# Kernel optimization log

Hardware: AMD Instinct MI355X
Metric: run time of the kernel (lower is better)

## Reference

```python
import jax, jax.numpy as jnp
import numpy as np

H = 128  # GRU hidden size

def gru_cell(x, h, Wih, Whh, bih, bhh):
    # torch GRU gate order: r, z, n
    gx = x @ Wih.T + bih          # (B, 3H)
    gh = h @ Whh.T + bhh          # (B, 3H)
    xr, xz, xn = jnp.split(gx, 3, axis=-1)
    hr, hz, hn = jnp.split(gh, 3, axis=-1)
    r = jax.nn.sigmoid(xr + hr)
    z = jax.nn.sigmoid(xz + hz)
    n = jnp.tanh(xn + r * hn)
    return (1.0 - z) * n + z * h

def conv2d(x, w, b, stride):
    y = jax.lax.conv_general_dilated(x, w, window_strides=(stride, stride), padding='VALID',
                                     dimension_numbers=('NCHW', 'OIHW', 'NCHW'))
    return y + b[None, :, None, None]

def setup_inputs() -> dict:
    key = jax.random.key(0)
    ks = jax.random.split(key, 20)
    B, T = 8192, 64
    s = lambda *sh: 0.1
    inp = {
        'cnn_states': jax.random.normal(ks[0], (B, 8, 8, 27), jnp.float32),
        'linears_states': jax.random.normal(ks[1], (B, T, 29), jnp.float32),
        'conv1_w': jax.random.normal(ks[2], (16, 27, 3, 3), jnp.float32) * 0.1,
        'conv1_b': jnp.zeros((16,), jnp.float32),
        'conv2_w': jax.random.normal(ks[3], (32, 16, 2, 2), jnp.float32) * 0.1,
        'conv2_b': jnp.zeros((32,), jnp.float32),
        'fc_w': jax.random.normal(ks[4], (128, 128), jnp.float32) * 0.1,
        'fc_b': jnp.zeros((128,), jnp.float32),
        'enc_Wih': jax.random.normal(ks[5], (3 * H, 29), jnp.float32) * 0.1,
        'enc_Whh': jax.random.normal(ks[6], (3 * H, H), jnp.float32) * 0.1,
        'enc_bih': jnp.zeros((3 * H,), jnp.float32),
        'enc_bhh': jnp.zeros((3 * H,), jnp.float32),
        'dec_Wih': jax.random.normal(ks[7], (3 * H, H), jnp.float32) * 0.1,
        'dec_Whh': jax.random.normal(ks[8], (3 * H, H), jnp.float32) * 0.1,
        'dec_bih': jnp.zeros((3 * H,), jnp.float32),
        'dec_bhh': jnp.zeros((3 * H,), jnp.float32),
        'dis_w': jax.random.normal(ks[9], (78, 256), jnp.float32) * 0.01,
        'dis_b': jnp.zeros((78,), jnp.float32),
        'value_w': jax.random.normal(ks[10], (1, 256), jnp.float32) * 0.1,
        'value_b': jnp.zeros((1,), jnp.float32),
    }
    return inp

def _forward(cnn_states, linears_states, conv1_w, conv1_b, conv2_w, conv2_b, fc_w, fc_b,
             enc_Wih, enc_Whh, enc_bih, enc_bhh, dec_Wih, dec_Whh, dec_bih, dec_bhh,
             dis_w, dis_b, value_w, value_b):
    B, T = linears_states.shape[0], linears_states.shape[1]
    # CNN encoder (NHWC -> NCHW)
    x = jnp.transpose(cnn_states, (0, 3, 1, 2))
    x = jax.nn.relu(conv2d(x, conv1_w, conv1_b, 2))   # (B,16,3,3)
    x = jax.nn.relu(conv2d(x, conv2_w, conv2_b, 1))   # (B,32,2,2)
    x = x.reshape(B, -1)                               # (B,128), CHW order matches torch Flatten
    z_cnn = jax.nn.relu(x @ fc_w.T + fc_b)             # (B,128)

    # encoder GRU over linears_states
    xs = jnp.transpose(linears_states, (1, 0, 2))      # (T,B,29)
    h0 = jnp.zeros((B, H), linears_states.dtype)
    def enc_step(h, xt):
        h2 = gru_cell(xt, h, enc_Wih, enc_Whh, enc_bih, enc_bhh)
        return h2, None
    h_enc, _ = jax.lax.scan(enc_step, h0, xs)

    x0 = jnp.zeros((B, H), linears_states.dtype)
    def dec_step(carry, _):
        xin, h = carry
        h2 = gru_cell(xin, h, dec_Wih, dec_Whh, dec_bih, dec_bhh)
        return (h2, h2), None
    (z_pn, _), _ = jax.lax.scan(dec_step, (x0, h_enc), None, length=T)

    pn = jnp.concatenate([z_cnn, z_pn], axis=1)        # (B,256)
    distris = pn @ dis_w.T + dis_b                     # (B,78)
    value = pn @ value_w.T + value_b                   # (B,1)
    return distris, value

def reference(cnn_states, linears_states, conv1_w, conv1_b, conv2_w, conv2_b, fc_w, fc_b,
              enc_Wih, enc_Whh, enc_bih, enc_bhh, dec_Wih, dec_Whh, dec_bih, dec_bhh,
              dis_w, dis_b, value_w, value_b):
    return _forward(cnn_states, linears_states, conv1_w, conv1_b, conv2_w, conv2_b, fc_w, fc_b,
                    enc_Wih, enc_Whh, enc_bih, enc_bhh, dec_Wih, dec_Whh, dec_bih, dec_bhh,
                    dis_w, dis_b, value_w, value_b)
```

## Files before the change

### kernel.cpp

```cpp
#include <hip/hip_runtime.h>

typedef _Float16 f16;
typedef _Float16 f16x8 __attribute__((ext_vector_type(8)));
typedef float f32x4 __attribute__((ext_vector_type(4)));

#define WS_EWIH 4194304
#define WS_EWHH 4218880
#define WS_DWC  4317184
#define WS_DWHH 4448256
#define WS_BIAS 4546560
#define WS_W1F  4550656
#define WS_W2F  4559872
#define WS_FCWF 4563968

static __device__ __forceinline__ f32x4 mfma16(f16x8 a, f16x8 b, f32x4 c) {
    return __builtin_amdgcn_mfma_f32_16x16x32_f16(a, b, c, 0, 0, 0);
}
static __device__ __forceinline__ float fexp2n(float x) {
    return __builtin_amdgcn_exp2f(x * -1.4426950408889634f);
}

__global__ void k_prep(const float* __restrict__ eWih, const float* __restrict__ eWhh,
                       const float* __restrict__ ebih, const float* __restrict__ ebhh,
                       const float* __restrict__ dWih, const float* __restrict__ dWhh,
                       const float* __restrict__ dbih, const float* __restrict__ dbhh,
                       const float* __restrict__ w1, const float* __restrict__ w2,
                       const float* __restrict__ fcw,
                       char* __restrict__ ws)
{
    f16* ewih = (f16*)(ws + WS_EWIH);
    f16* ewhh = (f16*)(ws + WS_EWHH);
    f16* dwc  = (f16*)(ws + WS_DWC);
    f16* dwhh = (f16*)(ws + WS_DWHH);
    float* bias = (float*)(ws + WS_BIAS);
    f16* w1f = (f16*)(ws + WS_W1F);
    f16* w2f = (f16*)(ws + WS_W2F);
    f16* fcwf = (f16*)(ws + WS_FCWF);
    const int total = 12288 + 49152 + 65536 + 49152 + 1024 + 4608 + 2048 + 16384;
    for (int i = blockIdx.x * 256 + threadIdx.x; i < total; i += gridDim.x * 256) {
        int j = i;
        if (j < 12288) { int g = j >> 5, k = j & 31;
            ewih[j] = (f16)((k < 29) ? eWih[g * 29 + k] : 0.0f); continue; }
        j -= 12288;
        if (j < 49152) { ewhh[j] = (f16)eWhh[j]; continue; }
        j -= 49152;
        if (j < 65536) { int row = j >> 7, k = j & 127; float v;
            if (row < 256)      v = dWih[row * 128 + k] + dWhh[row * 128 + k];
            else if (row < 384) v = dWih[row * 128 + k];
            else                v = dWhh[(row - 128) * 128 + k];
            dwc[j] = (f16)v; continue; }
        j -= 65536;
        if (j < 49152) { dwhh[j] = (f16)dWhh[j]; continue; }
        j -= 49152;
        if (j < 1024) {
            if (j < 256)        bias[j] = ebih[j] + ebhh[j];
            else if (j < 384)   bias[j] = ebih[j];
            else if (j < 512)   bias[j] = ebhh[j - 128];
            else if (j < 768)   bias[j] = dbih[j - 512] + dbhh[j - 512];
            else if (j < 896)   bias[j] = dbih[j - 512];
            else                bias[j] = dbhh[j - 640];
            continue; }
        j -= 1024;
        if (j < 4608) {
            int kk = j >> 9, rem = j & 511, co = rem >> 5, k = rem & 31;
            w1f[j] = (f16)((k < 27) ? w1[co * 243 + k * 9 + kk] : 0.0f); continue; }
        j -= 4608;
        if (j < 2048) {
            int s = j >> 10, rem = j & 1023, co = rem >> 5, k = rem & 31;
            int kk2 = 2 * s + (k >= 16), ci = k & 15;
            w2f[j] = (f16)w2[co * 64 + ci * 4 + kk2]; continue; }
        j -= 2048;
        fcwf[j] = (f16)fcw[j];
    }
}

__global__ __launch_bounds__(512, 2) void k_gru(
    const float* __restrict__ cin,
    const float* __restrict__ lin,
    const float* __restrict__ b1, const float* __restrict__ b2,
    const float* __restrict__ fcb,
    const char* __restrict__ ws,
    const float* __restrict__ dis_w, const float* __restrict__ dis_b,
    const float* __restrict__ value_w, const float* __restrict__ value_b,
    float* __restrict__ out)
{
    __shared__ __align__(16) char smem[55296];
    f16 (*h_s)[2][16][136]  = (f16(*)[2][16][136])(smem);
    f16 (*x_s)[2][16][32]   = (f16(*)[2][16][32])(smem + 17408);
    float (*pn_s)[264]      = (float(*)[264])(smem + 21504);
    f16 (*a1f)[9][24]       = (f16(*)[9][24])(smem);
    f16 (*vf)[136]          = (f16(*)[136])(smem + 8704);

    const int tid = threadIdx.x;
    const int wv = tid >> 6;
    const int lane = tid & 63;
    const int nl = lane & 15;
    const int quad = lane >> 4;
    const int j0 = wv * 16;
    const int row0 = blockIdx.x * 32;

    const f16* ewih = (const f16*)(ws + WS_EWIH);
    const f16* ewhh = (const f16*)(ws + WS_EWHH);
    const f16* dwc  = (const f16*)(ws + WS_DWC);
    const f16* dwhh = (const f16*)(ws + WS_DWHH);
    const float* bias = (const float*)(ws + WS_BIAS);
    const f16* w1f = (const f16*)(ws + WS_W1F);
    const f16* w2f = (const f16*)(ws + WS_W2F);
    const f16* fcwf = (const f16*)(ws + WS_FCWF);

    for (int g = 0; g < 2; g++) {
        const float* imgp = cin + (size_t)(row0 + g * 16 + nl) * 1728 + quad * 8;
        float b1v = b1[nl];
        for (int p = wv; p < 9; p += 8) {
            int oy = p / 3, ox = p % 3;
            f32x4 acc = {b1v, b1v, b1v, b1v};
            #pragma unroll
            for (int kk = 0; kk < 9; kk++) {
                f16x8 bw = *(const f16x8*)(w1f + (kk * 16 + nl) * 32 + quad * 8);
                int pix = (2 * oy + kk / 3) * 8 + (2 * ox + kk % 3);
                const float* s = imgp + pix * 27;
                f16x8 a;
                #pragma unroll
                for (int jj = 0; jj < 8; jj++) a[jj] = (f16)s[jj];
                acc = mfma16(a, bw, acc);
            }
            #pragma unroll
            for (int r = 0; r < 4; r++)
                a1f[quad * 4 + r][p][nl] = (f16)fmaxf(acc[r], 0.0f);
        }
        __syncthreads();
        {
            int pos = wv >> 1, nt = wv & 1;
            int y = pos >> 1, x = pos & 1;
            float bv = b2[nt * 16 + nl];
            f32x4 acc = {bv, bv, bv, bv};
            #pragma unroll
            for (int s = 0; s < 2; s++) {
                int kk2 = 2 * s + (quad >> 1);
                int pos1 = (y + (kk2 >> 1)) * 3 + (x + (kk2 & 1));
                f16x8 a = *(const f16x8*)(&a1f[nl][pos1][(quad & 1) * 8]);
                f16x8 b = *(const f16x8*)(w2f + ((size_t)s * 32 + nt * 16 + nl) * 32 + quad * 8);
                acc = mfma16(a, b, acc);
            }
            #pragma unroll
            for (int r = 0; r < 4; r++)
                vf[quad * 4 + r][(nt * 16 + nl) * 4 + (y * 2 + x)] = (f16)fmaxf(acc[r], 0.0f);
        }
        __syncthreads();
        {
            int o = wv * 16 + nl;
            float bv = fcb[o];
            f32x4 acc = {bv, bv, bv, bv};
            #pragma unroll
            for (int kt = 0; kt < 4; kt++) {
                f16x8 a = *(const f16x8*)(&vf[nl][kt * 32 + quad * 8]);
                f16x8 b = *(const f16x8*)(fcwf + o * 128 + kt * 32 + quad * 8);
                acc = mfma16(a, b, acc);
            }
            #pragma unroll
            for (int r = 0; r < 4; r++)
                pn_s[g * 16 + quad * 4 + r][o] = fmaxf(acc[r], 0.0f);
        }
        __syncthreads();
    }

    for (int i = tid; i < 2 * 2 * 16 * 136; i += 512) ((f16*)h_s)[i] = (f16)0.0f;

    const int rsw = (nl & 8) ? 16 : 0;
    const int wrow = quad * 4;
    const int wsw = (quad >= 2) ? 16 : 0;
    const int wcol = (j0 + nl + wsw) & 127;
    const int c0 = (quad * 8 + rsw) & 127;
    const int c1 = (32 + quad * 8 + rsw) & 127;
    const int c2 = (64 + quad * 8 + rsw) & 127;
    const int c3 = (96 + quad * 8 + rsw) & 127;

    float hoA[4], hoB[4];
    #pragma unroll
    for (int r = 0; r < 4; r++) { hoA[r] = 0.0f; hoB[r] = 0.0f; }

    const int xr = tid >> 5, xc = tid & 31;
    const bool xok = (xc < 29);
    const size_t lin_baseA = (size_t)(row0 + xr) * 1856 + xc;
    const size_t lin_baseB = (size_t)(row0 + 16 + xr) * 1856 + xc;

#define GATES(AR, AZ, AXN, AHN, HO, OB, TI, BR, BZ, BXN, BHN)                        \
        _Pragma("unroll")                                                            \
        for (int r = 0; r < 4; r++) {                                                \
            float ea = fexp2n((AR)[r]), eb = fexp2n((AZ)[r]);                        \
            float s1 = 1.0f + ea, s2 = 1.0f + eb;                                    \
            float R = __builtin_amdgcn_rcpf(s1 * s2);                                \
            float rg = s2 * R, zg = s1 * R;                                          \
            float ec = fexp2n(2.0f * ((AXN)[r] + rg * (AHN)[r]));                    \
            float ng = (1.0f - ec) * __builtin_amdgcn_rcpf(1.0f + ec);               \
            float h = ng + zg * ((HO)[r] - ng);                                      \
            (HO)[r] = h;                                                             \
            h_s[OB][TI][wrow + r][wcol] = (f16)h;                                    \
        }

    {
        float eb_r, eb_z, eb_xn, eb_hn;
        { int c = j0 + nl;
          eb_r = bias[c]; eb_z = bias[128 + c]; eb_xn = bias[256 + c]; eb_hn = bias[384 + c]; }
        f16x8 we_r[4], we_z[4], we_hn[4], we_xr, we_xz, we_xn;
        { int gr = j0 + nl;
          #pragma unroll
          for (int kt = 0; kt < 4; kt++) {
              we_r[kt]  = *(const f16x8*)(ewhh + gr * 128 + kt * 32 + quad * 8);
              we_z[kt]  = *(const f16x8*)(ewhh + (128 + gr) * 128 + kt * 32 + quad * 8);
              we_hn[kt] = *(const f16x8*)(ewhh + (256 + gr) * 128 + kt * 32 + quad * 8);
          }
          we_xr = *(const f16x8*)(ewih + gr * 32 + quad * 8);
          we_xz = *(const f16x8*)(ewih + (128 + gr) * 32 + quad * 8);
          we_xn = *(const f16x8*)(ewih + (256 + gr) * 32 + quad * 8);
        }

        float xvA = xok ? lin[lin_baseA] : 0.0f;
        float xvB = xok ? lin[lin_baseB] : 0.0f;

#define ENC_STEP(BUF, OBUF, TN)                                                      \
        do {                                                                         \
            x_s[BUF][0][xr][xc] = (f16)xvA;                                          \
            x_s[BUF][1][xr][xc] = (f16)xvB;                                          \
            __syncthreads();                                                         \
            f16x8 axA = *(const f16x8*)(&x_s[BUF][0][nl][quad * 8]);                 \
            f16x8 axB = *(const f16x8*)(&x_s[BUF][1][nl][quad * 8]);                 \
            f16x8 aA0 = *(const f16x8*)(&h_s[BUF][0][nl][c0]);                       \
            f16x8 aA1 = *(const f16x8*)(&h_s[BUF][0][nl][c1]);                       \
            f16x8 aA2 = *(const f16x8*)(&h_s[BUF][0][nl][c2]);                       \
            f16x8 aA3 = *(const f16x8*)(&h_s[BUF][0][nl][c3]);                       \
            f16x8 aB0 = *(const f16x8*)(&h_s[BUF][1][nl][c0]);                       \
            f16x8 aB1 = *(const f16x8*)(&h_s[BUF][1][nl][c1]);                       \
            f16x8 aB2 = *(const f16x8*)(&h_s[BUF][1][nl][c2]);                       \
            f16x8 aB3 = *(const f16x8*)(&h_s[BUF][1][nl][c3]);                       \
            if ((TN) < 64) {                                                         \
                xvA = xok ? lin[lin_baseA + (TN) * 29] : 0.0f;                       \
                xvB = xok ? lin[lin_baseB + (TN) * 29] : 0.0f;                       \
            }                                                                        \
            f32x4 aRA  = {eb_r, eb_r, eb_r, eb_r},   aRB  = aRA;                     \
            f32x4 aZA  = {eb_z, eb_z, eb_z, eb_z},   aZB  = aZA;                     \
            f32x4 aXNA = {eb_xn, eb_xn, eb_xn, eb_xn}, aXNB = aXNA;                  \
            f32x4 aHNA = {eb_hn, eb_hn, eb_hn, eb_hn}, aHNB = aHNA;                  \
            aRA  = mfma16(axA, we_xr, aRA);   aRB  = mfma16(axB, we_xr, aRB);        \
            aZA  = mfma16(axA, we_xz, aZA);   aZB  = mfma16(axB, we_xz, aZB);        \
            aXNA = mfma16(axA, we_xn, aXNA);  aXNB = mfma16(axB, we_xn, aXNB);       \
            aRA  = mfma16(aA0, we_r[0], aRA);  aRB  = mfma16(aB0, we_r[0], aRB);     \
            aRA  = mfma16(aA1, we_r[1], aRA);  aRB  = mfma16(aB1, we_r[1], aRB);     \
            aRA  = mfma16(aA2, we_r[2], aRA);  aRB  = mfma16(aB2, we_r[2], aRB);     \
            aRA  = mfma16(aA3, we_r[3], aRA);  aRB  = mfma16(aB3, we_r[3], aRB);     \
            aZA  = mfma16(aA0, we_z[0], aZA);  aZB  = mfma16(aB0, we_z[0], aZB);     \
            aZA  = mfma16(aA1, we_z[1], aZA);  aZB  = mfma16(aB1, we_z[1], aZB);     \
            aZA  = mfma16(aA2, we_z[2], aZA);  aZB  = mfma16(aB2, we_z[2], aZB);     \
            aZA  = mfma16(aA3, we_z[3], aZA);  aZB  = mfma16(aB3, we_z[3], aZB);     \
            aHNA = mfma16(aA0, we_hn[0], aHNA); aHNB = mfma16(aB0, we_hn[0], aHNB);  \
            aHNA = mfma16(aA1, we_hn[1], aHNA); aHNB = mfma16(aB1, we_hn[1], aHNB);  \
            aHNA = mfma16(aA2, we_hn[2], aHNA); aHNB = mfma16(aB2, we_hn[2], aHNB);  \
            aHNA = mfma16(aA3, we_hn[3], aHNA); aHNB = mfma16(aB3, we_hn[3], aHNB);  \
            GATES(aRA, aZA, aXNA, aHNA, hoA, OBUF, 0, , , , )                        \
            GATES(aRB, aZB, aXNB, aHNB, hoB, OBUF, 1, , , , )                        \
        } while (0)

        for (int t = 0; t < 64; t += 2) {
            ENC_STEP(0, 1, t + 1);
            ENC_STEP(1, 0, t + 2);
        }
#undef ENC_STEP
    }

    float db_r, db_z, db_xn, db_hn;
    { int c = j0 + nl;
      db_r = bias[512 + c]; db_z = bias[640 + c]; db_xn = bias[768 + c]; db_hn = bias[896 + c]; }

    {
        __syncthreads();
        f16x8 aA0 = *(const f16x8*)(&h_s[0][0][nl][c0]);
        f16x8 aA1 = *(const f16x8*)(&h_s[0][0][nl][c1]);
        f16x8 aA2 = *(const f16x8*)(&h_s[0][0][nl][c2]);
        f16x8 aA3 = *(const f16x8*)(&h_s[0][0][nl][c3]);
        f16x8 aB0 = *(const f16x8*)(&h_s[0][1][nl][c0]);
        f16x8 aB1 = *(const f16x8*)(&h_s[0][1][nl][c1]);
        f16x8 aB2 = *(const f16x8*)(&h_s[0][1][nl][c2]);
        f16x8 aB3 = *(const f16x8*)(&h_s[0][1][nl][c3]);
        int gr = j0 + nl;
        f32x4 aRA  = {db_r, db_r, db_r, db_r},   aRB  = aRA;
        f32x4 aZA  = {db_z, db_z, db_z, db_z},   aZB  = aZA;
        f32x4 aHNA = {db_hn, db_hn, db_hn, db_hn}, aHNB = aHNA;
        #pragma unroll
        for (int kt = 0; kt < 4; kt++) {
            f16x8 b0 = *(const f16x8*)(dwhh + gr * 128 + kt * 32 + quad * 8);
            f16x8 b1 = *(const f16x8*)(dwhh + (128 + gr) * 128 + kt * 32 + quad * 8);
            f16x8 b2 = *(const f16x8*)(dwhh + (256 + gr) * 128 + kt * 32 + quad * 8);
            f16x8 aA = (kt == 0) ? aA0 : (kt == 1) ? aA1 : (kt == 2) ? aA2 : aA3;
            f16x8 aB = (kt == 0) ? aB0 : (kt == 1) ? aB1 : (kt == 2) ? aB2 : aB3;
            aRA  = mfma16(aA, b0, aRA);   aRB  = mfma16(aB, b0, aRB);
            aZA  = mfma16(aA, b1, aZA);   aZB  = mfma16(aB, b1, aZB);
            aHNA = mfma16(aA, b2, aHNA);  aHNB = mfma16(aB, b2, aHNB);
        }
        #pragma unroll
        for (int r = 0; r < 4; r++) {
            float ea = fexp2n(aRA[r]), eb = fexp2n(aZA[r]);
            float s1 = 1.0f + ea, s2 = 1.0f + eb;
            float R = __builtin_amdgcn_rcpf(s1 * s2);
            float rg = s2 * R, zg = s1 * R;
            float ec = fexp2n(2.0f * (db_xn + rg * aHNA[r]));
            float ng = (1.0f - ec) * __builtin_amdgcn_rcpf(1.0f + ec);
            float h = ng + zg * (hoA[r] - ng);
            hoA[r] = h;
            h_s[1][0][wrow + r][wcol] = (f16)h;
        }
        #pragma unroll
        for (int r = 0; r < 4; r++) {
            float ea = fexp2n(aRB[r]), eb = fexp2n(aZB[r]);
            float s1 = 1.0f + ea, s2 = 1.0f + eb;
            float R = __builtin_amdgcn_rcpf(s1 * s2);
            float rg = s2 * R, zg = s1 * R;
            float ec = fexp2n(2.0f * (db_xn + rg * aHNB[r]));
            float ng = (1.0f - ec) * __builtin_amdgcn_rcpf(1.0f + ec);
            float h = ng + zg * (hoB[r] - ng);
            hoB[r] = h;
            h_s[1][1][wrow + r][wcol] = (f16)h;
        }
    }
    {
        f16x8 wd_r[4], wd_z[4], wd_xn[4], wd_hn[4];
        { int gr = j0 + nl;
          #pragma unroll
          for (int kt = 0; kt < 4; kt++) {
              wd_r[kt]  = *(const f16x8*)(dwc + gr * 128 + kt * 32 + quad * 8);
              wd_z[kt]  = *(const f16x8*)(dwc + (128 + gr) * 128 + kt * 32 + quad * 8);
              wd_xn[kt] = *(const f16x8*)(dwc + (256 + gr) * 128 + kt * 32 + quad * 8);
              wd_hn[kt] = *(const f16x8*)(dwc + (384 + gr) * 128 + kt * 32 + quad * 8);
          }
        }

#define DEC_STEP(BUF, OBUF)                                                          \
        do {                                                                         \
            __syncthreads();                                                         \
            f16x8 aA0 = *(const f16x8*)(&h_s[BUF][0][nl][c0]);                       \
            f16x8 aA1 = *(const f16x8*)(&h_s[BUF][0][nl][c1]);                       \
            f16x8 aA2 = *(const f16x8*)(&h_s[BUF][0][nl][c2]);                       \
            f16x8 aA3 = *(const f16x8*)(&h_s[BUF][0][nl][c3]);                       \
            f16x8 aB0 = *(const f16x8*)(&h_s[BUF][1][nl][c0]);                       \
            f16x8 aB1 = *(const f16x8*)(&h_s[BUF][1][nl][c1]);                       \
            f16x8 aB2 = *(const f16x8*)(&h_s[BUF][1][nl][c2]);                       \
            f16x8 aB3 = *(const f16x8*)(&h_s[BUF][1][nl][c3]);                       \
            f32x4 aRA  = {db_r, db_r, db_r, db_r},   aRB  = aRA;                     \
            f32x4 aZA  = {db_z, db_z, db_z, db_z},   aZB  = aZA;                     \
            f32x4 aXNA = {db_xn, db_xn, db_xn, db_xn}, aXNB = aXNA;                  \
            f32x4 aHNA = {db_hn, db_hn, db_hn, db_hn}, aHNB = aHNA;                  \
            aRA  = mfma16(aA0, wd_r[0], aRA);   aRB  = mfma16(aB0, wd_r[0], aRB);    \
            aRA  = mfma16(aA1, wd_r[1], aRA);   aRB  = mfma16(aB1, wd_r[1], aRB);    \
            aRA  = mfma16(aA2, wd_r[2], aRA);   aRB  = mfma16(aB2, wd_r[2], aRB);    \
            aRA  = mfma16(aA3, wd_r[3], aRA);   aRB  = mfma16(aB3, wd_r[3], aRB);    \
            aZA  = mfma16(aA0, wd_z[0], aZA);   aZB  = mfma16(aB0, wd_z[0], aZB);    \
            aZA  = mfma16(aA1, wd_z[1], aZA);   aZB  = mfma16(aB1, wd_z[1], aZB);    \
            aZA  = mfma16(aA2, wd_z[2], aZA);   aZB  = mfma16(aB2, wd_z[2], aZB);    \
            aZA  = mfma16(aA3, wd_z[3], aZA);   aZB  = mfma16(aB3, wd_z[3], aZB);    \
            aXNA = mfma16(aA0, wd_xn[0], aXNA); aXNB = mfma16(aB0, wd_xn[0], aXNB);  \
            aXNA = mfma16(aA1, wd_xn[1], aXNA); aXNB = mfma16(aB1, wd_xn[1], aXNB);  \
            aXNA = mfma16(aA2, wd_xn[2], aXNA); aXNB = mfma16(aB2, wd_xn[2], aXNB);  \
            aXNA = mfma16(aA3, wd_xn[3], aXNA); aXNB = mfma16(aB3, wd_xn[3], aXNB);  \
            aHNA = mfma16(aA0, wd_hn[0], aHNA); aHNB = mfma16(aB0, wd_hn[0], aHNB);  \
            aHNA = mfma16(aA1, wd_hn[1], aHNA); aHNB = mfma16(aB1, wd_hn[1], aHNB);  \
            aHNA = mfma16(aA2, wd_hn[2], aHNA); aHNB = mfma16(aB2, wd_hn[2], aHNB);  \
            aHNA = mfma16(aA3, wd_hn[3], aHNA); aHNB = mfma16(aB3, wd_hn[3], aHNB);  \
            GATES(aRA, aZA, aXNA, aHNA, hoA, OBUF, 0, , , , )                        \
            GATES(aRB, aZB, aXNB, aHNB, hoB, OBUF, 1, , , , )                        \
        } while (0)

        DEC_STEP(1, 0);
        for (int t = 2; t < 64; t += 2) {
            DEC_STEP(0, 1);
            DEC_STEP(1, 0);
        }
#undef DEC_STEP
#undef GATES
    }

    #pragma unroll
    for (int r = 0; r < 4; r++) {
        pn_s[wrow + r][128 + j0 + nl] = hoA[r];
        pn_s[16 + wrow + r][128 + j0 + nl] = hoB[r];
    }
    __syncthreads();

    const int rr = tid & 31, og = tid >> 5;
    const float4* pr4 = (const float4*)(&pn_s[rr][0]);
    for (int o = og; o < 79; o += 16) {
        const float* wrow_p = (o < 78) ? (dis_w + o * 256) : value_w;
        float acc = (o < 78) ? dis_b[o] : value_b[0];
        const float4* wr4 = (const float4*)wrow_p;
        #pragma unroll 8
        for (int k = 0; k < 64; k++) {
            float4 a = wr4[k], b = pr4[k];
            acc += a.x * b.x + a.y * b.y + a.z * b.z + a.w * b.w;
        }
        if (o < 78) out[(size_t)(row0 + rr) * 78 + o] = acc;
        else        out[(size_t)8192 * 78 + row0 + rr] = acc;
    }
}

extern "C" void kernel_launch(void* const* d_in, const int* in_sizes, int n_in,
                              void* d_out, int out_size, void* d_ws, size_t ws_size,
                              hipStream_t stream)
{
    (void)in_sizes; (void)n_in; (void)out_size; (void)ws_size;
    const float* cnn  = (const float*)d_in[0];
    const float* lin  = (const float*)d_in[1];
    const float* c1w  = (const float*)d_in[2];
    const float* c1b  = (const float*)d_in[3];
    const float* c2w  = (const float*)d_in[4];
    const float* c2b  = (const float*)d_in[5];
    const float* fcw  = (const float*)d_in[6];
    const float* fcb  = (const float*)d_in[7];
    const float* eWih = (const float*)d_in[8];
    const float* eWhh = (const float*)d_in[9];
    const float* ebih = (const float*)d_in[10];
    const float* ebhh = (const float*)d_in[11];
    const float* dWih = (const float*)d_in[12];
    const float* dWhh = (const float*)d_in[13];
    const float* dbih = (const float*)d_in[14];
    const float* dbhh = (const float*)d_in[15];
    const float* disw = (const float*)d_in[16];
    const float* disb = (const float*)d_in[17];
    const float* vw   = (const float*)d_in[18];
    const float* vb   = (const float*)d_in[19];
    char* ws = (char*)d_ws;
    float* out = (float*)d_out;

    hipLaunchKernelGGL(k_prep, dim3(128), dim3(256), 0, stream,
                       eWih, eWhh, ebih, ebhh, dWih, dWhh, dbih, dbhh,
                       c1w, c2w, fcw, ws);
    hipLaunchKernelGGL(k_gru, dim3(256), dim3(512), 0, stream,
                       cnn, lin, c1b, c2b, fcb, ws, disw, disb, vw, vb, out);
}
```

Measured before the change: 348.1 us.

## Stage GRU recurrent weights in swizzled dynamic LDS and spill CNN features

```diff
diff --git a/kernel.cpp b/kernel.cpp
--- a/kernel.cpp
+++ b/kernel.cpp
@@ -4,6 +4,7 @@
 typedef _Float16 f16x8 __attribute__((ext_vector_type(8)));
 typedef float f32x4 __attribute__((ext_vector_type(4)));
 
+#define WS_ZCNN 0
 #define WS_EWIH 4194304
 #define WS_EWHH 4218880
 #define WS_DWC  4317184
@@ -18,6 +19,17 @@
 }
 static __device__ __forceinline__ float fexp2n(float x) {
     return __builtin_amdgcn_exp2f(x * -1.4426950408889634f);
+}
+
+static __device__ __forceinline__ void copy_w_lds(const f16* __restrict__ src,
+                                                  char* __restrict__ dst,
+                                                  int rows, int tid)
+{
+    for (int c = tid, e = rows * 16; c < e; c += 512) {
+        int row = c >> 4, slot = c & 15;
+        *(f16x8*)(dst + row * 256 + ((slot * 16) ^ ((row & 7) << 4))) =
+            *(const f16x8*)(src + row * 128 + slot * 8);
+    }
 }
 
 __global__ void k_prep(const float* __restrict__ eWih, const float* __restrict__ eWhh,
@@ -79,17 +91,17 @@
     const float* __restrict__ lin,
     const float* __restrict__ b1, const float* __restrict__ b2,
     const float* __restrict__ fcb,
-    const char* __restrict__ ws,
+    char* __restrict__ ws,
     const float* __restrict__ dis_w, const float* __restrict__ dis_b,
     const float* __restrict__ value_w, const float* __restrict__ value_b,
     float* __restrict__ out)
 {
-    __shared__ __align__(16) char smem[55296];
+    __shared__ __align__(16) char smem[21504];
     f16 (*h_s)[2][16][136]  = (f16(*)[2][16][136])(smem);
     f16 (*x_s)[2][16][32]   = (f16(*)[2][16][32])(smem + 17408);
-    float (*pn_s)[264]      = (float(*)[264])(smem + 21504);
     f16 (*a1f)[9][24]       = (f16(*)[9][24])(smem);
     f16 (*vf)[136]          = (f16(*)[136])(smem + 8704);
+    extern __shared__ __align__(16) char wlds[];
 
     const int tid = threadIdx.x;
     const int wv = tid >> 6;
@@ -98,6 +110,9 @@
     const int quad = lane >> 4;
     const int j0 = wv * 16;
     const int row0 = blockIdx.x * 32;
+    const int wswz = (nl & 7) << 4;
+
+#define WREAD(ROW, KT) (*(const f16x8*)(wlds + (ROW) * 256 + ((((KT) * 64) + quad * 16) ^ wswz)))
 
     const f16* ewih = (const f16*)(ws + WS_EWIH);
     const f16* ewhh = (const f16*)(ws + WS_EWHH);
@@ -107,6 +122,9 @@
     const f16* w1f = (const f16*)(ws + WS_W1F);
     const f16* w2f = (const f16*)(ws + WS_W2F);
     const f16* fcwf = (const f16*)(ws + WS_FCWF);
+    float* zc = (float*)(ws + WS_ZCNN);
+
+    copy_w_lds(ewhh, wlds, 384, tid);
 
     for (int g = 0; g < 2; g++) {
         const float* imgp = cin + (size_t)(row0 + g * 16 + nl) * 1728 + quad * 8;
@@ -159,7 +177,7 @@
             }
             #pragma unroll
             for (int r = 0; r < 4; r++)
-                pn_s[g * 16 + quad * 4 + r][o] = fmaxf(acc[r], 0.0f);
+                zc[(size_t)(row0 + g * 16 + quad * 4 + r) * 128 + o] = fmaxf(acc[r], 0.0f);
         }
         __syncthreads();
     }
@@ -184,7 +202,7 @@
     const size_t lin_baseA = (size_t)(row0 + xr) * 1856 + xc;
     const size_t lin_baseB = (size_t)(row0 + 16 + xr) * 1856 + xc;
 
-#define GATES(AR, AZ, AXN, AHN, HO, OB, TI, BR, BZ, BXN, BHN)                        \
+#define GATES(AR, AZ, AXN, AHN, HO, OB, TI)                                          \
         _Pragma("unroll")                                                            \
         for (int r = 0; r < 4; r++) {                                                \
             float ea = fexp2n((AR)[r]), eb = fexp2n((AZ)[r]);                        \
@@ -206,9 +224,9 @@
         { int gr = j0 + nl;
           #pragma unroll
           for (int kt = 0; kt < 4; kt++) {
-              we_r[kt]  = *(const f16x8*)(ewhh + gr * 128 + kt * 32 + quad * 8);
-              we_z[kt]  = *(const f16x8*)(ewhh + (128 + gr) * 128 + kt * 32 + quad * 8);
-              we_hn[kt] = *(const f16x8*)(ewhh + (256 + gr) * 128 + kt * 32 + quad * 8);
+              we_r[kt]  = WREAD(gr, kt);
+              we_z[kt]  = WREAD(128 + gr, kt);
+              we_hn[kt] = WREAD(256 + gr, kt);
           }
           we_xr = *(const f16x8*)(ewih + gr * 32 + quad * 8);
           we_xz = *(const f16x8*)(ewih + (128 + gr) * 32 + quad * 8);
@@ -256,8 +274,8 @@
             aHNA = mfma16(aA1, we_hn[1], aHNA); aHNB = mfma16(aB1, we_hn[1], aHNB);  \
             aHNA = mfma16(aA2, we_hn[2], aHNA); aHNB = mfma16(aB2, we_hn[2], aHNB);  \
             aHNA = mfma16(aA3, we_hn[3], aHNA); aHNB = mfma16(aB3, we_hn[3], aHNB);  \
-            GATES(aRA, aZA, aXNA, aHNA, hoA, OBUF, 0, , , , )                        \
-            GATES(aRB, aZB, aXNB, aHNB, hoB, OBUF, 1, , , , )                        \
+            GATES(aRA, aZA, aXNA, aHNA, hoA, OBUF, 0)                                \
+            GATES(aRB, aZB, aXNB, aHNB, hoB, OBUF, 1)                                \
         } while (0)
 
         for (int t = 0; t < 64; t += 2) {
@@ -271,8 +289,10 @@
     { int c = j0 + nl;
       db_r = bias[512 + c]; db_z = bias[640 + c]; db_xn = bias[768 + c]; db_hn = bias[896 + c]; }
 
+    __syncthreads();
+    copy_w_lds(dwc, wlds, 512, tid);
+
     {
-        __syncthreads();
         f16x8 aA0 = *(const f16x8*)(&h_s[0][0][nl][c0]);
         f16x8 aA1 = *(const f16x8*)(&h_s[0][0][nl][c1]);
         f16x8 aA2 = *(const f16x8*)(&h_s[0][0][nl][c2]);
@@ -326,10 +346,10 @@
         { int gr = j0 + nl;
           #pragma unroll
           for (int kt = 0; kt < 4; kt++) {
-              wd_r[kt]  = *(const f16x8*)(dwc + gr * 128 + kt * 32 + quad * 8);
-              wd_z[kt]  = *(const f16x8*)(dwc + (128 + gr) * 128 + kt * 32 + quad * 8);
-              wd_xn[kt] = *(const f16x8*)(dwc + (256 + gr) * 128 + kt * 32 + quad * 8);
-              wd_hn[kt] = *(const f16x8*)(dwc + (384 + gr) * 128 + kt * 32 + quad * 8);
+              wd_r[kt]  = WREAD(gr, kt);
+              wd_z[kt]  = WREAD(128 + gr, kt);
+              wd_xn[kt] = WREAD(256 + gr, kt);
+              wd_hn[kt] = WREAD(384 + gr, kt);
           }
         }
 
@@ -364,8 +384,8 @@
             aHNA = mfma16(aA1, wd_hn[1], aHNA); aHNB = mfma16(aB1, wd_hn[1], aHNB);  \
             aHNA = mfma16(aA2, wd_hn[2], aHNA); aHNB = mfma16(aB2, wd_hn[2], aHNB);  \
             aHNA = mfma16(aA3, wd_hn[3], aHNA); aHNB = mfma16(aB3, wd_hn[3], aHNB);  \
-            GATES(aRA, aZA, aXNA, aHNA, hoA, OBUF, 0, , , , )                        \
-            GATES(aRB, aZB, aXNB, aHNB, hoB, OBUF, 1, , , , )                        \
+            GATES(aRA, aZA, aXNA, aHNA, hoA, OBUF, 0)                                \
+            GATES(aRB, aZB, aXNB, aHNB, hoB, OBUF, 1)                                \
         } while (0)
 
         DEC_STEP(1, 0);
@@ -377,15 +397,22 @@
 #undef GATES
     }
 
+    __syncthreads();
+    float (*pn)[264] = (float(*)[264])wlds;
+    for (int i = tid; i < 32 * 32; i += 512) {
+        int row = i >> 5, c4 = i & 31;
+        *(float4*)(&pn[row][c4 * 4]) =
+            *(const float4*)(zc + (size_t)(row0 + row) * 128 + c4 * 4);
+    }
     #pragma unroll
     for (int r = 0; r < 4; r++) {
-        pn_s[wrow + r][128 + j0 + nl] = hoA[r];
-        pn_s[16 + wrow + r][128 + j0 + nl] = hoB[r];
+        pn[wrow + r][128 + j0 + nl] = hoA[r];
+        pn[16 + wrow + r][128 + j0 + nl] = hoB[r];
     }
     __syncthreads();
 
     const int rr = tid & 31, og = tid >> 5;
-    const float4* pr4 = (const float4*)(&pn_s[rr][0]);
+    const float4* pr4 = (const float4*)(&pn[rr][0]);
     for (int o = og; o < 79; o += 16) {
         const float* wrow_p = (o < 78) ? (dis_w + o * 256) : value_w;
         float acc = (o < 78) ? dis_b[o] : value_b[0];
@@ -398,6 +425,7 @@
         if (o < 78) out[(size_t)(row0 + rr) * 78 + o] = acc;
         else        out[(size_t)8192 * 78 + row0 + rr] = acc;
     }
+#undef WREAD
 }
 
 extern "C" void kernel_launch(void* const* d_in, const int* in_sizes, int n_in,
@@ -431,6 +459,6 @@
     hipLaunchKernelGGL(k_prep, dim3(128), dim3(256), 0, stream,
                        eWih, eWhh, ebih, ebhh, dWih, dWhh, dbih, dbhh,
                        c1w, c2w, fcw, ws);
-    hipLaunchKernelGGL(k_gru, dim3(256), dim3(512), 0, stream,
+    hipLaunchKernelGGL(k_gru, dim3(256), dim3(512), 131072, stream,
                        cnn, lin, c1b, c2b, fcb, ws, disw, disb, vw, vb, out);
 }
```

New measurement: 347.5 us. Within noise of the previous version (-0.2%).
